# Performance work log

Measured on AMD Instinct MI355X. Metric: run time of the kernel, lower is better.

Reference implementation:

```python
import jax, jax.numpy as jnp
import numpy as np
import math

N_HEADS = 16
D_KV = 64
NUM_BUCKETS = 32
MAX_DISTANCE = 128


def _rel_bucket(rel_pos, num_buckets=NUM_BUCKETS, max_distance=MAX_DISTANCE):
    # bidirectional=True branch of relative_position_bucket
    n = -rel_pos
    num_buckets //= 2
    ret = (n < 0).astype(jnp.int32) * num_buckets
    n = jnp.abs(n)
    max_exact = num_buckets // 2
    is_small = n < max_exact
    val_large = max_exact + (
        jnp.log(n.astype(jnp.float32) / max_exact)
        / math.log(max_distance / max_exact)
        * (num_buckets - max_exact)
    ).astype(jnp.int32)
    val_large = jnp.minimum(val_large, num_buckets - 1)
    return jnp.where(is_small, n, val_large) + ret


def setup_inputs() -> dict:
    key = jax.random.key(0)
    ks = jax.random.split(key, 6)
    T, D = 2048, 1024
    x = jax.random.normal(ks[0], (T, D), dtype=jnp.float32)
    Wq = jax.random.normal(ks[1], (D, N_HEADS * D_KV), dtype=jnp.float32) * 0.02
    Wk = jax.random.normal(ks[2], (D, N_HEADS * D_KV), dtype=jnp.float32) * 0.02
    Wv = jax.random.normal(ks[3], (D, N_HEADS * D_KV), dtype=jnp.float32) * 0.02
    Wo = jax.random.normal(ks[4], (N_HEADS * D_KV, D), dtype=jnp.float32) * 0.02
    rel_bias_table = jax.random.normal(ks[5], (NUM_BUCKETS, N_HEADS), dtype=jnp.float32) * 0.02
    q_lens = jnp.full((4,), 512, dtype=jnp.int32)  # packed varlen: 4 seqs of 512, sum == T
    return {"x": x, "Wq": Wq, "Wk": Wk, "Wv": Wv, "Wo": Wo,
            "rel_bias_table": rel_bias_table, "q_lens": q_lens}


def _attention(x, Wq, Wk, Wv, Wo, rel_bias_table, q_lens):
    T = x.shape[0]
    q = x @ Wq
    k = x @ Wk
    v = x @ Wv
    to_heads = lambda t: jnp.transpose(t.reshape(T, N_HEADS, D_KV), (1, 0, 2))  # [H,T,d]
    q_h, k_h, v_h = to_heads(q), to_heads(k), to_heads(v)

    # fp32 scores (no 1/sqrt(d) scaling in T5; module uses scaling=1.0)
    scores = jnp.einsum('hqd,hkd->hqk', q_h.astype(jnp.float32), k_h.astype(jnp.float32))

    # sequence ids / positions within packed layout
    starts = jnp.cumsum(q_lens, dtype=jnp.int32) - q_lens
    indicators = jnp.zeros(T, dtype=jnp.int32).at[starts].set(1)
    seq_ids = jnp.cumsum(indicators, dtype=jnp.int32) - 1
    pos = jnp.arange(T) - starts[seq_ids]

    # relative position bias (encoder: bidirectional)
    rel_pos = pos[None, :] - pos[:, None]  # [T,T]
    buckets = _rel_bucket(rel_pos)
    bias = jnp.transpose(rel_bias_table[buckets], (2, 0, 1))  # [H,T,T]
    scores = scores + bias.astype(jnp.float32)

    # block-diagonal mask over packed sequences (non-causal encoder)
    total = jnp.sum(q_lens)
    valid = jnp.arange(T) < total
    mask = (seq_ids[:, None] == seq_ids[None, :]) & valid[:, None] & valid[None, :]
    scores = jnp.where(mask[None], scores, jnp.finfo(scores.dtype).min)

    weights = jax.nn.softmax(scores, axis=-1)
    out = jnp.einsum('hqk,hkd->hqd', weights, v_h.astype(jnp.float32))
    out = jnp.transpose(out, (1, 0, 2)).reshape(T, N_HEADS * D_KV)
    return out.astype(x.dtype) @ Wo


def reference(x, Wq, Wk, Wv, Wo, rel_bias_table, q_lens):
    return _attention(x, Wq, Wk, Wv, Wo, rel_bias_table, q_lens)
```

## Files before the change

### kernel.cpp

```cpp
#include <hip/hip_runtime.h>

#define NH 16

typedef __bf16 bf16x8 __attribute__((ext_vector_type(8)));
typedef unsigned short u16x8 __attribute__((ext_vector_type(8)));
typedef float f32x4 __attribute__((ext_vector_type(4)));
typedef unsigned short u16;

__device__ __forceinline__ u16 f2bu(float f) {
    unsigned int u = __builtin_bit_cast(unsigned int, f);
    u = (u + 0x7FFFu + ((u >> 16) & 1u)) >> 16;
    return (u16)u;
}
__device__ __forceinline__ bf16x8 ld_bf8(const u16* p) {
    return __builtin_bit_cast(bf16x8, *(const u16x8*)p);
}
__device__ __forceinline__ void gl_lds16(const void* g, void* l) {
    __builtin_amdgcn_global_load_lds((const __attribute__((address_space(1))) void*)g,
                                     (__attribute__((address_space(3))) void*)l, 16, 0, 0);
}

__device__ __forceinline__ int rel_bucket(int delta) {
    int n = -delta;
    int ret = (n < 0) ? 16 : 0;
    int na = n < 0 ? -n : n;
    int b;
    if (na < 8) b = na;
    else if (na < 12) b = 8;
    else if (na < 16) b = 9;
    else if (na < 23) b = 10;
    else if (na < 32) b = 11;
    else if (na < 46) b = 12;
    else if (na < 64) b = 13;
    else if (na < 91) b = 14;
    else b = 15;
    return b + ret;
}

#define L2E 1.4426950408889634f

__global__ void prep_all(const float* __restrict__ x, u16* __restrict__ xb, int n,
                         const float* __restrict__ Wq, const float* __restrict__ Wk,
                         const float* __restrict__ Wv, const float* __restrict__ Wo,
                         u16* __restrict__ Wt, u16* __restrict__ Wot, int cb) {
    __shared__ float tile[32][33];
    int b = blockIdx.x, tid = threadIdx.x;
    if (b < cb) {
        int i = (b * 256 + tid) * 4;
        if (i >= n) return;
        float4 v = *(const float4*)&x[i];
        u16 o0 = f2bu(v.x), o1 = f2bu(v.y), o2 = f2bu(v.z), o3 = f2bu(v.w);
        xb[i] = o0; xb[i+1] = o1; xb[i+2] = o2; xb[i+3] = o3;
    } else {
        int t = b - cb;
        int z = t >> 10; t &= 1023;
        const float* src = z == 0 ? Wq : z == 1 ? Wk : z == 2 ? Wv : Wo;
        u16* dst = z < 3 ? Wt + (size_t)z * 1024 * 1024 : Wot;
        int r0 = (t >> 5) * 32, c0 = (t & 31) * 32;
        int tx = tid & 31, ty = tid >> 5;
        #pragma unroll
        for (int i = 0; i < 32; i += 8)
            tile[ty + i][tx] = src[(size_t)(r0 + ty + i) * 1024 + c0 + tx];
        __syncthreads();
        #pragma unroll
        for (int i = 0; i < 32; i += 8)
            dst[(size_t)(c0 + ty + i) * 1024 + r0 + tx] = f2bu(tile[tx][ty + i]);
    }
}

template<int MODE, int BM, int XR, int XC>
__global__ __launch_bounds__(256)
void gemm_bt(const u16* __restrict__ A, const u16* __restrict__ Bt,
             int N, int K, int T,
             float* __restrict__ Cf, u16* __restrict__ qkb, u16* __restrict__ vtb) {
    constexpr int MI = BM / 32;
    constexpr int STG = (BM + 128) * 64;
    constexpr int LDSN = (MODE == 1 && 128 * 136 > STG) ? 128 * 136 : STG;
    __shared__ __attribute__((aligned(16))) u16 lds[LDSN];
    const int tid = threadIdx.x;
    const int l = tid & 63, wv = tid >> 6;
    const int l16 = l & 15, lg = l >> 4;
    const int lrow = l >> 3, lslot = l & 7;
    const int wm = (wv >> 1) * (BM / 2), wn = (wv & 1) * 64;

    int bmi, bni;
    {
        int gx = gridDim.x, gy = gridDim.y;
        int lin = blockIdx.y * gx + blockIdx.x;
        int nrx = gx / XR, nrc = gy / XC;
        if (gx % XR == 0 && gy % XC == 0 && nrx * nrc == 8) {
            int xcd = lin & 7, loc = lin >> 3;
            int rr = xcd / nrc, rc = xcd % nrc;
            bmi = rr * XR + (loc % XR);
            bni = rc * XC + (loc / XR);
        } else { bmi = blockIdx.x; bni = blockIdx.y; }
    }
    const int bm = bmi * BM, bn = bni * 128;

    f32x4 acc[MI][4];
    #pragma unroll
    for (int i = 0; i < MI; i++)
        #pragma unroll
        for (int j = 0; j < 4; j++)
            #pragma unroll
            for (int r = 0; r < 4; r++) acc[i][j][r] = 0.f;

    u16* As_ = lds;
    u16* Bs_ = lds + BM * 64;
    for (int k0 = 0; k0 < K; k0 += 64) {
        __syncthreads();
        #pragma unroll
        for (int c = 0; c < MI; ++c) {
            int chunk = c * 4 + wv;
            int row = chunk * 8 + lrow;
            int gs = lslot ^ (row & 7);
            gl_lds16(&A[(size_t)(bm + row) * K + k0 + gs * 8], &As_[chunk * 512]);
        }
        #pragma unroll
        for (int c = 0; c < 4; ++c) {
            int chunk = c * 4 + wv;
            int row = chunk * 8 + lrow;
            int gs = lslot ^ (row & 7);
            gl_lds16(&Bt[(size_t)(bn + row) * K + k0 + gs * 8], &Bs_[chunk * 512]);
        }
        __syncthreads();
        #pragma unroll
        for (int kk = 0; kk < 2; ++kk) {
            bf16x8 af[MI], bfv[4];
            #pragma unroll
            for (int i = 0; i < MI; i++) {
                int row = wm + i * 16 + l16;
                af[i] = ld_bf8(&As_[row * 64 + (((kk * 4 + lg) ^ (row & 7)) * 8)]);
            }
            #pragma unroll
            for (int j = 0; j < 4; j++) {
                int row = wn + j * 16 + l16;
                bfv[j] = ld_bf8(&Bs_[row * 64 + (((kk * 4 + lg) ^ (row & 7)) * 8)]);
            }
            #pragma unroll
            for (int i = 0; i < MI; i++)
                #pragma unroll
                for (int j = 0; j < 4; j++)
                    acc[i][j] = __builtin_amdgcn_mfma_f32_16x16x32_bf16(af[i], bfv[j], acc[i][j], 0, 0, 0);
        }
    }

    if (MODE == 0) {
        #pragma unroll
        for (int i = 0; i < MI; i++)
            #pragma unroll
            for (int j = 0; j < 4; j++) {
                int col = bn + wn + j * 16 + l16;
                #pragma unroll
                for (int r = 0; r < 4; r++) {
                    int row = bm + wm + i * 16 + lg * 4 + r;
                    Cf[(size_t)row * N + col] = acc[i][j][r];
                }
            }
    } else if (bn < 2048) {
        #pragma unroll
        for (int i = 0; i < MI; i++)
            #pragma unroll
            for (int j = 0; j < 4; j++) {
                int col = bn + wn + j * 16 + l16;
                #pragma unroll
                for (int r = 0; r < 4; r++) {
                    int row = bm + wm + i * 16 + lg * 4 + r;
                    qkb[(size_t)row * 2048 + col] = f2bu(acc[i][j][r]);
                }
            }
    } else {
        __syncthreads();
        #pragma unroll
        for (int i = 0; i < MI; i++)
            #pragma unroll
            for (int j = 0; j < 4; j++) {
                int cl = wn + j * 16 + l16;
                #pragma unroll
                for (int r = 0; r < 4; r++)
                    lds[cl * 136 + wm + i * 16 + lg * 4 + r] = f2bu(acc[i][j][r]);
            }
        __syncthreads();
        int cl = tid >> 1, hf = tid & 1;
        size_t gb = (size_t)(bn - 2048 + cl) * T + bm + hf * 64;
        #pragma unroll
        for (int k2 = 0; k2 < 8; ++k2) {
            int4 v4 = *(const int4*)&lds[cl * 136 + hf * 64 + k2 * 8];
            *(int4*)&vtb[gb + k2 * 8] = v4;
        }
    }
}

__global__ __launch_bounds__(256)
void attn_kernel(const u16* __restrict__ qkb, const u16* __restrict__ vtb,
                 const float* __restrict__ tbl, const int* __restrict__ q_lens, int nseq,
                 u16* __restrict__ attnb, int T) {
    __shared__ __attribute__((aligned(16))) u16 KV[2][2][4096];
    __shared__ __attribute__((aligned(16))) u16 Ps[4][16][72];
    __shared__ float biasLds[2112];
    const int tid = threadIdx.x;
    const int l = tid & 63, wv = tid >> 6;
    const int l16 = l & 15, lg = l >> 4;
    const int lrow = l >> 3, lslot = l & 7;

    int nbk = gridDim.x * gridDim.y;
    int lin = blockIdx.y * gridDim.x + blockIdx.x;
    int lin2 = (nbk & 7) ? lin : (lin & 7) * (nbk >> 3) + (lin >> 3);
    const int h = lin2 / gridDim.x;
    const int q0 = (lin2 % gridDim.x) * 64;

    int cums[9]; cums[0] = 0;
    #pragma unroll
    for (int i = 0; i < 8; ++i) cums[i + 1] = cums[i] + (i < nseq ? q_lens[i] : 0);
    auto seq_of = [&](int t) -> int {
        int s = -1;
        #pragma unroll
        for (int i = 0; i < 8; ++i)
            if (t >= cums[i] && t < cums[i + 1]) s = i;
        return s;
    };
    const int s0 = seq_of(q0), s1 = seq_of(q0 + 63);
    const bool uni = (s0 == s1) && (s0 >= 0);
    const int kvA = uni ? cums[s0] : 0;
    const int kvB = uni ? cums[s0 + 1] : T;
    const int len = kvB - kvA;

    for (int t = tid; t < len + 64; t += 256)
        biasLds[t] = tbl[rel_bucket(kvA - q0 - 63 + t) * NH + h] * L2E;

    bf16x8 qf[2];
    {
        int tq = q0 + wv * 16 + l16;
        const u16* qp = qkb + (size_t)tq * 2048 + h * 64 + lg * 8;
        qf[0] = ld_bf8(qp); qf[1] = ld_bf8(qp + 32);
    }
    int tqr[4], sqr[4];
    #pragma unroll
    for (int r = 0; r < 4; r++) {
        tqr[r] = q0 + wv * 16 + lg * 4 + r;
        sqr[r] = uni ? s0 : seq_of(tqr[r]);
    }

    const u16* kg = qkb + 1024 + h * 64;
    const u16* vg = vtb + (size_t)(h * 64) * T;
    auto stage = [&](int base, int bi) {
        #pragma unroll
        for (int c = 0; c < 2; ++c) {
            int chunk = c * 4 + wv;
            int row = chunk * 8 + lrow;
            int gs = lslot ^ (row & 7);
            int tk = base + row; if (tk > T - 1) tk = T - 1;
            gl_lds16(kg + (size_t)tk * 2048 + gs * 8, &KV[bi][0][chunk * 512]);
            gl_lds16(vg + (size_t)row * T + base + gs * 8, &KV[bi][1][chunk * 512]);
        }
    };

    float psum[4] = {0.f, 0.f, 0.f, 0.f};
    f32x4 o[4];
    #pragma unroll
    for (int d = 0; d < 4; d++)
        #pragma unroll
        for (int r = 0; r < 4; r++) o[d][r] = 0.f;

    stage(kvA, 0);
    __syncthreads();
    int cur = 0;
    for (int base = kvA; base < kvB; base += 64) {
        if (base + 64 < kvB) stage(base + 64, cur ^ 1);
        const u16* Kb = KV[cur][0];
        const u16* Vb = KV[cur][1];

        f32x4 s[4];
        #pragma unroll
        for (int kt = 0; kt < 4; kt++)
            #pragma unroll
            for (int r = 0; r < 4; r++) s[kt][r] = 0.f;
        #pragma unroll
        for (int kk = 0; kk < 2; kk++)
            #pragma unroll
            for (int kt = 0; kt < 4; kt++) {
                int rw = kt * 16 + l16;
                bf16x8 kf = ld_bf8(Kb + rw * 64 + (((kk * 4 + lg) ^ (rw & 7)) * 8));
                s[kt] = __builtin_amdgcn_mfma_f32_16x16x32_bf16(qf[kk], kf, s[kt], 0, 0, 0);
            }

        const int cbi = (base - kvA) + 63 + l16 - wv * 16 - lg * 4;
        if (uni && base + 64 <= kvB) {
            #pragma unroll
            for (int r = 0; r < 4; r++) {
                const float* bp = &biasLds[cbi - r];
                #pragma unroll
                for (int kt = 0; kt < 4; kt++) {
                    float p = __builtin_amdgcn_exp2f(__builtin_fmaf(s[kt][r], L2E, bp[kt * 16]));
                    psum[r] += p;
                    Ps[wv][lg * 4 + r][kt * 16 + l16] = f2bu(p);
                }
            }
        } else {
            int skt[4];
            #pragma unroll
            for (int kt = 0; kt < 4; kt++) {
                int tk = base + kt * 16 + l16;
                skt[kt] = (tk < T) ? (uni ? s0 : seq_of(tk)) : -2;
            }
            #pragma unroll
            for (int r = 0; r < 4; r++) {
                const float* bp = &biasLds[cbi - r];
                #pragma unroll
                for (int kt = 0; kt < 4; kt++) {
                    float p = __builtin_amdgcn_exp2f(__builtin_fmaf(s[kt][r], L2E, bp[kt * 16]));
                    if (uni) {
                        int tk = base + kt * 16 + l16;
                        if (tk >= kvB) p = 0.f;
                    } else {
                        bool ok = (skt[kt] >= 0) && (skt[kt] == sqr[r]);
                        p = (sqr[r] < 0) ? 1.f : (ok ? p : 0.f);
                    }
                    psum[r] += p;
                    Ps[wv][lg * 4 + r][kt * 16 + l16] = f2bu(p);
                }
            }
        }
        bf16x8 pf0 = ld_bf8(&Ps[wv][l16][lg * 8]);
        bf16x8 pf1 = ld_bf8(&Ps[wv][l16][32 + lg * 8]);
        #pragma unroll
        for (int kk = 0; kk < 2; kk++) {
            bf16x8 pf = kk ? pf1 : pf0;
            #pragma unroll
            for (int dt = 0; dt < 4; dt++) {
                int rw = dt * 16 + l16;
                bf16x8 vf = ld_bf8(Vb + rw * 64 + (((kk * 4 + lg) ^ (rw & 7)) * 8));
                o[dt] = __builtin_amdgcn_mfma_f32_16x16x32_bf16(pf, vf, o[dt], 0, 0, 0);
            }
        }
        __syncthreads();
        cur ^= 1;
    }

    float lsum[4];
    #pragma unroll
    for (int r = 0; r < 4; r++) {
        float v = psum[r];
        #pragma unroll
        for (int m = 1; m < 16; m <<= 1) v += __shfl_xor(v, m, 64);
        lsum[r] = v;
    }
    #pragma unroll
    for (int dt = 0; dt < 4; dt++)
        #pragma unroll
        for (int r = 0; r < 4; r++)
            attnb[(size_t)tqr[r] * 1024 + h * 64 + dt * 16 + l16] = f2bu(o[dt][r] / lsum[r]);
}

extern "C" void kernel_launch(void* const* d_in, const int* in_sizes, int n_in,
                              void* d_out, int out_size, void* d_ws, size_t ws_size,
                              hipStream_t stream) {
    const float* x   = (const float*)d_in[0];
    const float* Wq  = (const float*)d_in[1];
    const float* Wk  = (const float*)d_in[2];
    const float* Wv  = (const float*)d_in[3];
    const float* Wo  = (const float*)d_in[4];
    const float* tbl = (const float*)d_in[5];
    const int* q_lens = (const int*)d_in[6];
    const int T = in_sizes[0] / 1024;
    const int nseq = in_sizes[6];

    char* ws = (char*)d_ws;
    auto alloc = [&](size_t bytes) { char* p = ws; ws += (bytes + 255) & ~(size_t)255; return p; };
    u16*   xb    = (u16*)alloc((size_t)T * 1024 * 2);
    u16*   Wt    = (u16*)alloc((size_t)3072 * 1024 * 2);
    u16*   Wot   = (u16*)alloc((size_t)1024 * 1024 * 2);
    u16*   qkb   = (u16*)alloc((size_t)T * 2048 * 2);
    u16*   vtb   = (u16*)alloc((size_t)1024 * T * 2);
    u16*   attnb = (u16*)alloc((size_t)T * 1024 * 2);

    int cb = (T * 1024 / 4 + 255) / 256;
    prep_all<<<dim3(cb + 4096), dim3(256), 0, stream>>>(
        x, xb, T * 1024, Wq, Wk, Wv, Wo, Wt, Wot, cb);

    gemm_bt<1, 128, 8, 6><<<dim3(T / 128, 3072 / 128), dim3(256), 0, stream>>>(
        xb, Wt, 3072, 1024, T, nullptr, qkb, vtb);
    attn_kernel<<<dim3(T / 64, NH), dim3(256), 0, stream>>>(
        qkb, vtb, tbl, q_lens, nseq, attnb, T);
    gemm_bt<0, 64, 8, 4><<<dim3(T / 64, 1024 / 128), dim3(256), 0, stream>>>(
        attnb, Wot, 1024, 1024, T, (float*)d_out, nullptr, nullptr);
}
```

Measured before the change: 137.3 us.

## Double-buffer GEMM LDS staging; load attention K/V directly into registers

The projection GEMM now double-buffers its LDS tiles, prefetching the next K-slice while the current one is multiplied, which removes one barrier per iteration. The attention kernel drops LDS staging of K and V. Each wave loads its MFMA operands straight from global memory into registers, with a software-pipelined prefetch of the next K tile, and raises wave priority around the MFMA blocks. This trades LDS traffic and barriers for more global loads per wave, since each wave re-reads K and V, plus higher register pressure and LDS use in the GEMM.

Result: slower. 147.7 us (+7.6%).

```diff
diff --git a/kernel.cpp b/kernel.cpp
--- a/kernel.cpp
+++ b/kernel.cpp
@@ -14,6 +14,9 @@
 }
 __device__ __forceinline__ bf16x8 ld_bf8(const u16* p) {
     return __builtin_bit_cast(bf16x8, *(const u16x8*)p);
+}
+__device__ __forceinline__ bf16x8 i4bf(const int4 v) {
+    return __builtin_bit_cast(bf16x8, v);
 }
 __device__ __forceinline__ void gl_lds16(const void* g, void* l) {
     __builtin_amdgcn_global_load_lds((const __attribute__((address_space(1))) void*)g,
@@ -75,7 +78,7 @@
              float* __restrict__ Cf, u16* __restrict__ qkb, u16* __restrict__ vtb) {
     constexpr int MI = BM / 32;
     constexpr int STG = (BM + 128) * 64;
-    constexpr int LDSN = (MODE == 1 && 128 * 136 > STG) ? 128 * 136 : STG;
+    constexpr int LDSN = (MODE == 1 && 128 * 136 > 2 * STG) ? 128 * 136 : 2 * STG;
     __shared__ __attribute__((aligned(16))) u16 lds[LDSN];
     const int tid = threadIdx.x;
     const int l = tid & 63, wv = tid >> 6;
@@ -105,10 +108,9 @@
             #pragma unroll
             for (int r = 0; r < 4; r++) acc[i][j][r] = 0.f;
 
-    u16* As_ = lds;
-    u16* Bs_ = lds + BM * 64;
-    for (int k0 = 0; k0 < K; k0 += 64) {
-        __syncthreads();
+    auto stage = [&](int k0, int bi) {
+        u16* As_ = lds + bi * STG;
+        u16* Bs_ = As_ + BM * 64;
         #pragma unroll
         for (int c = 0; c < MI; ++c) {
             int chunk = c * 4 + wv;
@@ -123,19 +125,27 @@
             int gs = lslot ^ (row & 7);
             gl_lds16(&Bt[(size_t)(bn + row) * K + k0 + gs * 8], &Bs_[chunk * 512]);
         }
-        __syncthreads();
+    };
+
+    stage(0, 0);
+    __syncthreads();
+    int cur = 0;
+    for (int k0 = 0; k0 < K; k0 += 64) {
+        if (k0 + 64 < K) stage(k0 + 64, cur ^ 1);
+        const u16* As = lds + cur * STG;
+        const u16* Bs = As + BM * 64;
         #pragma unroll
         for (int kk = 0; kk < 2; ++kk) {
             bf16x8 af[MI], bfv[4];
             #pragma unroll
             for (int i = 0; i < MI; i++) {
                 int row = wm + i * 16 + l16;
-                af[i] = ld_bf8(&As_[row * 64 + (((kk * 4 + lg) ^ (row & 7)) * 8)]);
+                af[i] = ld_bf8(&As[row * 64 + (((kk * 4 + lg) ^ (row & 7)) * 8)]);
             }
             #pragma unroll
             for (int j = 0; j < 4; j++) {
                 int row = wn + j * 16 + l16;
-                bfv[j] = ld_bf8(&Bs_[row * 64 + (((kk * 4 + lg) ^ (row & 7)) * 8)]);
+                bfv[j] = ld_bf8(&Bs[row * 64 + (((kk * 4 + lg) ^ (row & 7)) * 8)]);
             }
             #pragma unroll
             for (int i = 0; i < MI; i++)
@@ -143,6 +153,8 @@
                 for (int j = 0; j < 4; j++)
                     acc[i][j] = __builtin_amdgcn_mfma_f32_16x16x32_bf16(af[i], bfv[j], acc[i][j], 0, 0, 0);
         }
+        __syncthreads();
+        cur ^= 1;
     }
 
     if (MODE == 0) {
@@ -170,7 +182,6 @@
                 }
             }
     } else {
-        __syncthreads();
         #pragma unroll
         for (int i = 0; i < MI; i++)
             #pragma unroll
@@ -195,13 +206,11 @@
 void attn_kernel(const u16* __restrict__ qkb, const u16* __restrict__ vtb,
                  const float* __restrict__ tbl, const int* __restrict__ q_lens, int nseq,
                  u16* __restrict__ attnb, int T) {
-    __shared__ __attribute__((aligned(16))) u16 KV[2][2][4096];
     __shared__ __attribute__((aligned(16))) u16 Ps[4][16][72];
     __shared__ float biasLds[2112];
     const int tid = threadIdx.x;
     const int l = tid & 63, wv = tid >> 6;
     const int l16 = l & 15, lg = l >> 4;
-    const int lrow = l >> 3, lslot = l & 7;
 
     int nbk = gridDim.x * gridDim.y;
     int lin = blockIdx.y * gridDim.x + blockIdx.x;
@@ -240,20 +249,10 @@
         tqr[r] = q0 + wv * 16 + lg * 4 + r;
         sqr[r] = uni ? s0 : seq_of(tqr[r]);
     }
+    __syncthreads();
 
     const u16* kg = qkb + 1024 + h * 64;
     const u16* vg = vtb + (size_t)(h * 64) * T;
-    auto stage = [&](int base, int bi) {
-        #pragma unroll
-        for (int c = 0; c < 2; ++c) {
-            int chunk = c * 4 + wv;
-            int row = chunk * 8 + lrow;
-            int gs = lslot ^ (row & 7);
-            int tk = base + row; if (tk > T - 1) tk = T - 1;
-            gl_lds16(kg + (size_t)tk * 2048 + gs * 8, &KV[bi][0][chunk * 512]);
-            gl_lds16(vg + (size_t)row * T + base + gs * 8, &KV[bi][1][chunk * 512]);
-        }
-    };
 
     float psum[4] = {0.f, 0.f, 0.f, 0.f};
     f32x4 o[4];
@@ -262,27 +261,37 @@
         #pragma unroll
         for (int r = 0; r < 4; r++) o[d][r] = 0.f;
 
-    stage(kvA, 0);
-    __syncthreads();
-    int cur = 0;
-    for (int base = kvA; base < kvB; base += 64) {
-        if (base + 64 < kvB) stage(base + 64, cur ^ 1);
-        const u16* Kb = KV[cur][0];
-        const u16* Vb = KV[cur][1];
-
+    auto ldK = [&](int base, int4* kr) {
+        #pragma unroll
+        for (int kt = 0; kt < 4; ++kt) {
+            int tk = base + kt * 16 + l16; if (tk > T - 1) tk = T - 1;
+            const u16* p = kg + (size_t)tk * 2048 + lg * 8;
+            kr[kt * 2 + 0] = *(const int4*)p;
+            kr[kt * 2 + 1] = *(const int4*)(p + 32);
+        }
+    };
+    auto ldV = [&](int base, int4* vr) {
+        #pragma unroll
+        for (int dt = 0; dt < 4; ++dt) {
+            const u16* p = vg + (size_t)(dt * 16 + l16) * T + base + lg * 8;
+            vr[dt * 2 + 0] = *(const int4*)p;
+            vr[dt * 2 + 1] = *(const int4*)(p + 32);
+        }
+    };
+
+    auto compute = [&](int base, const int4* kr, const int4* vr) {
         f32x4 s[4];
         #pragma unroll
         for (int kt = 0; kt < 4; kt++)
             #pragma unroll
             for (int r = 0; r < 4; r++) s[kt][r] = 0.f;
-        #pragma unroll
-        for (int kk = 0; kk < 2; kk++)
-            #pragma unroll
-            for (int kt = 0; kt < 4; kt++) {
-                int rw = kt * 16 + l16;
-                bf16x8 kf = ld_bf8(Kb + rw * 64 + (((kk * 4 + lg) ^ (rw & 7)) * 8));
-                s[kt] = __builtin_amdgcn_mfma_f32_16x16x32_bf16(qf[kk], kf, s[kt], 0, 0, 0);
-            }
+        __builtin_amdgcn_s_setprio(1);
+        #pragma unroll
+        for (int kt = 0; kt < 4; kt++) {
+            s[kt] = __builtin_amdgcn_mfma_f32_16x16x32_bf16(qf[0], i4bf(kr[kt * 2 + 0]), s[kt], 0, 0, 0);
+            s[kt] = __builtin_amdgcn_mfma_f32_16x16x32_bf16(qf[1], i4bf(kr[kt * 2 + 1]), s[kt], 0, 0, 0);
+        }
+        __builtin_amdgcn_s_setprio(0);
 
         const int cbi = (base - kvA) + 63 + l16 - wv * 16 - lg * 4;
         if (uni && base + 64 <= kvB) {
@@ -310,8 +319,7 @@
                 for (int kt = 0; kt < 4; kt++) {
                     float p = __builtin_amdgcn_exp2f(__builtin_fmaf(s[kt][r], L2E, bp[kt * 16]));
                     if (uni) {
-                        int tk = base + kt * 16 + l16;
-                        if (tk >= kvB) p = 0.f;
+                        if (base + kt * 16 + l16 >= kvB) p = 0.f;
                     } else {
                         bool ok = (skt[kt] >= 0) && (skt[kt] == sqr[r]);
                         p = (sqr[r] < 0) ? 1.f : (ok ? p : 0.f);
@@ -323,18 +331,26 @@
         }
         bf16x8 pf0 = ld_bf8(&Ps[wv][l16][lg * 8]);
         bf16x8 pf1 = ld_bf8(&Ps[wv][l16][32 + lg * 8]);
-        #pragma unroll
-        for (int kk = 0; kk < 2; kk++) {
-            bf16x8 pf = kk ? pf1 : pf0;
-            #pragma unroll
-            for (int dt = 0; dt < 4; dt++) {
-                int rw = dt * 16 + l16;
-                bf16x8 vf = ld_bf8(Vb + rw * 64 + (((kk * 4 + lg) ^ (rw & 7)) * 8));
-                o[dt] = __builtin_amdgcn_mfma_f32_16x16x32_bf16(pf, vf, o[dt], 0, 0, 0);
-            }
-        }
-        __syncthreads();
-        cur ^= 1;
+        __builtin_amdgcn_s_setprio(1);
+        #pragma unroll
+        for (int dt = 0; dt < 4; dt++) {
+            o[dt] = __builtin_amdgcn_mfma_f32_16x16x32_bf16(pf0, i4bf(vr[dt * 2 + 0]), o[dt], 0, 0, 0);
+            o[dt] = __builtin_amdgcn_mfma_f32_16x16x32_bf16(pf1, i4bf(vr[dt * 2 + 1]), o[dt], 0, 0, 0);
+        }
+        __builtin_amdgcn_s_setprio(0);
+    };
+
+    int4 krA[8], krB[8], vr[8];
+    ldK(kvA, krA);
+    for (int base = kvA; base < kvB; base += 128) {
+        ldV(base, vr);
+        if (base + 64 < kvB) ldK(base + 64, krB);
+        compute(base, krA, vr);
+        if (base + 64 < kvB) {
+            ldV(base + 64, vr);
+            if (base + 128 < kvB) ldK(base + 128, krA);
+            compute(base + 64, krB, vr);
+        }
     }
 
     float lsum[4];
```
